# Performance work log

Hardware: AMD Instinct MI355X
Metric: run time of the kernel (lower is better)

Reference implementation:

```python
import jax, jax.numpy as jnp
import numpy as np

B, D, rL, rD, d = 512, 960, 16, 32, 512
LP, LH = 16, 384
R_PH = 0.7
dP = int(round(R_PH * d))  # 358
dH = d - dP                # 154
BN_EPS = 1e-5


def _xavier(key, shape):
    limit = float(np.sqrt(6.0 / (shape[0] + shape[1])))
    return jax.random.uniform(key, shape, jnp.float32, -limit, limit)


def _prefix_mask(key, batch, L_pad):
    # contiguous prefix masks: Lb uniform in [1, L_pad]
    lens = jax.random.randint(key, (batch,), 1, L_pad + 1)
    return (jnp.arange(L_pad)[None, :] < lens[:, None]).astype(jnp.int32)


def setup_inputs() -> dict:
    key = jax.random.key(0)
    ks = jax.random.split(key, 24)
    inp = {
        "emb_P": jax.random.normal(ks[0], (B, LP, D), jnp.float32),
        "emb_H": jax.random.normal(ks[1], (B, LH, D), jnp.float32),
        "mask_P": _prefix_mask(ks[2], B, LP),
        "mask_H": _prefix_mask(ks[3], B, LH),
        # peptide encoder params
        "B_cP": _xavier(ks[4], (D, rD)),
        "A_cP": _xavier(ks[5], (LP, rL)),
        "H_cP": _xavier(ks[6], (rL * rD, dP)),
        "W1P": _xavier(ks[7], (dP, dP)), "b1P": jnp.zeros((dP,), jnp.float32),
        "gP": jnp.ones((dP,), jnp.float32), "betaP": jnp.zeros((dP,), jnp.float32),
        "W2P": _xavier(ks[8], (dP, dP)), "b2P": jnp.zeros((dP,), jnp.float32),
        # HLA encoder params
        "B_cH": _xavier(ks[9], (D, rD)),
        "A_cH": _xavier(ks[10], (LH, rL)),
        "H_cH": _xavier(ks[11], (rL * rD, dH)),
        "W1H": _xavier(ks[12], (dH, dH)), "b1H": jnp.zeros((dH,), jnp.float32),
        "gH": jnp.ones((dH,), jnp.float32), "betaH": jnp.zeros((dH,), jnp.float32),
        "W2H": _xavier(ks[13], (dH, dH)), "b2H": jnp.zeros((dH,), jnp.float32),
    }
    return inp


def _encode(emb, mask, B_c, A_c, H_c, W1, b1, g, beta, W2, b2):
    # masked low-rank projection; equivalent to the per-sample ragged loop
    # for contiguous prefix masks (A_c rows align with padded positions).
    Xm = emb * mask[..., None].astype(emb.dtype)            # (B, L, D)
    Y = jnp.einsum("bld,dr->blr", Xm, B_c)                  # (B, L, rD)
    U = jnp.einsum("lp,blr->bpr", A_c, Y)                   # (B, rL, rD)
    z = U.reshape(U.shape[0], -1) @ H_c                     # (B, d_mod)
    # expander (eval mode: BN uses running stats mean=0/var=1; dropout off)
    h = z @ W1 + b1
    h = h * (g / jnp.sqrt(1.0 + BN_EPS)) + beta
    h = jax.nn.relu(h)
    return h @ W2 + b2


def reference(emb_P, emb_H, B_cP, A_cP, H_cP, W1P, b1P, gP, betaP, W2P, b2P,
              B_cH, A_cH, H_cH, W1H, b1H, gH, betaH, W2H, b2H,
              mask_P, mask_H):
    zP = _encode(emb_P, mask_P, B_cP, A_cP, H_cP, W1P, b1P, gP, betaP, W2P, b2P)
    zH = _encode(emb_H, mask_H, B_cH, A_cH, H_cH, W1H, b1H, gH, betaH, W2H, b2H)
    return jnp.concatenate([zP, zH], axis=-1)  # (B, d)
```

## Files before the change

kernel.cpp:

```cpp
#include <hip/hip_runtime.h>
#include <cstddef>

constexpr int Bn  = 512;
constexpr int Dd  = 960;
constexpr int RL  = 16;
constexpr int RD  = 32;
constexpr int LPp = 16;
constexpr int LHh = 384;
constexpr int DP  = 358;
constexpr int DH  = 154;

typedef float f32x4 __attribute__((ext_vector_type(4)));

struct EncParams {
    const float* X;
    const int*   mask;
    const float* A;
    const float* Bc;
    const float* Hc;
    const float* W1;
    const float* b1;
    const float* g;
    const float* beta;
    const float* W2;
    const float* b2;
    int L;
    int dmod;
    int ooff;
};

__global__ __launch_bounds__(256)
void fused_kernel(EncParams H, EncParams P, float* __restrict__ out)
{
    const bool isH = ((int)blockIdx.x < Bn);
    const EncParams E = isH ? H : P;
    const int b = isH ? blockIdx.x : blockIdx.x - Bn;
    const int t = threadIdx.x;

    __shared__ float Vs[RL][Dd];
    __shared__ float Ush[RL * RD];
    __shared__ int   s_len;

    if (t == 0) s_len = 0;
    __syncthreads();
    int loc = 0;
    for (int i = t; i < E.L; i += 256) loc += E.mask[(size_t)b * E.L + i];
    if (loc) atomicAdd(&s_len, loc);
    __syncthreads();
    const int len = s_len;

    if (t < 240) {
        float v[RL][4];
        #pragma unroll
        for (int p = 0; p < RL; ++p)
            #pragma unroll
            for (int q = 0; q < 4; ++q) v[p][q] = 0.f;

        const float* xrow = E.X + (size_t)b * E.L * Dd + 4 * t;
        #pragma unroll 2
        for (int l = 0; l < len; ++l) {
            f32x4 xv = __builtin_nontemporal_load((const f32x4*)xrow);
            xrow += Dd;
            float a[RL];
            *(f32x4*)&a[0]  = *(const f32x4*)(E.A + (size_t)l * RL + 0);
            *(f32x4*)&a[4]  = *(const f32x4*)(E.A + (size_t)l * RL + 4);
            *(f32x4*)&a[8]  = *(const f32x4*)(E.A + (size_t)l * RL + 8);
            *(f32x4*)&a[12] = *(const f32x4*)(E.A + (size_t)l * RL + 12);
            #pragma unroll
            for (int p = 0; p < RL; ++p) {
                v[p][0] = fmaf(a[p], xv[0], v[p][0]);
                v[p][1] = fmaf(a[p], xv[1], v[p][1]);
                v[p][2] = fmaf(a[p], xv[2], v[p][2]);
                v[p][3] = fmaf(a[p], xv[3], v[p][3]);
            }
        }
        #pragma unroll
        for (int p = 0; p < RL; ++p)
            *(f32x4*)&Vs[p][4 * t] = *(f32x4*)&v[p][0];
    }
    __syncthreads();

    {
        const int p = t >> 5, r = t & 31;
        float u0 = 0.f, u1 = 0.f;
        for (int dd = 0; dd < Dd; dd += 4) {
            f32x4 v0 = *(const f32x4*)&Vs[p][dd];
            f32x4 v1 = *(const f32x4*)&Vs[p + 8][dd];
            #pragma unroll
            for (int q = 0; q < 4; ++q) {
                float bc = E.Bc[(size_t)(dd + q) * RD + r];
                u0 = fmaf(v0[q], bc, u0);
                u1 = fmaf(v1[q], bc, u1);
            }
        }
        Ush[p * RD + r]       = u0;
        Ush[(p + 8) * RD + r] = u1;
    }
    __syncthreads();

    float* zs = &Vs[0][0];
    float* hs = &Vs[0][0] + 512;
    for (int j = t; j < E.dmod; j += 256) {
        float acc = 0.f;
        #pragma unroll 8
        for (int i = 0; i < RL * RD; ++i)
            acc = fmaf(Ush[i], E.Hc[(size_t)i * E.dmod + j], acc);
        zs[j] = acc;
    }
    __syncthreads();

    const float bscale = rsqrtf(1.f + 1e-5f);
    for (int c = t; c < E.dmod; c += 256) {
        float acc = E.b1[c];
        #pragma unroll 4
        for (int k = 0; k < E.dmod; ++k)
            acc = fmaf(zs[k], E.W1[(size_t)k * E.dmod + c], acc);
        acc = fmaf(acc, E.g[c] * bscale, E.beta[c]);
        hs[c] = fmaxf(acc, 0.f);
    }
    __syncthreads();

    for (int c = t; c < E.dmod; c += 256) {
        float acc = E.b2[c];
        #pragma unroll 4
        for (int k = 0; k < E.dmod; ++k)
            acc = fmaf(hs[k], E.W2[(size_t)k * E.dmod + c], acc);
        out[(size_t)b * (DP + DH) + E.ooff + c] = acc;
    }
}

extern "C" void kernel_launch(void* const* d_in, const int* in_sizes, int n_in,
                              void* d_out, int out_size, void* d_ws, size_t ws_size,
                              hipStream_t stream)
{
    EncParams P, H;
    P.X    = (const float*)d_in[0];
    H.X    = (const float*)d_in[1];
    P.mask = (const int*)  d_in[2];
    H.mask = (const int*)  d_in[3];
    P.Bc   = (const float*)d_in[4];
    P.A    = (const float*)d_in[5];
    P.Hc   = (const float*)d_in[6];
    P.W1   = (const float*)d_in[7];
    P.b1   = (const float*)d_in[8];
    P.g    = (const float*)d_in[9];
    P.beta = (const float*)d_in[10];
    P.W2   = (const float*)d_in[11];
    P.b2   = (const float*)d_in[12];
    H.Bc   = (const float*)d_in[13];
    H.A    = (const float*)d_in[14];
    H.Hc   = (const float*)d_in[15];
    H.W1   = (const float*)d_in[16];
    H.b1   = (const float*)d_in[17];
    H.g    = (const float*)d_in[18];
    H.beta = (const float*)d_in[19];
    H.W2   = (const float*)d_in[20];
    H.b2   = (const float*)d_in[21];
    P.L = LPp;  P.dmod = DP;  P.ooff = 0;
    H.L = LHh;  H.dmod = DH;  H.ooff = DP;

    float* outp = (float*)d_out;

    fused_kernel<<<dim3(2 * Bn), dim3(256), 0, stream>>>(H, P, outp);
}
```

Measured before the change: 249.2 us.

## Split sequence reduction into segmented kernel with workspace partials and tail kernel

```diff
diff --git a/kernel.cpp b/kernel.cpp
--- a/kernel.cpp
+++ b/kernel.cpp
@@ -9,36 +9,95 @@
 constexpr int LHh = 384;
 constexpr int DP  = 358;
 constexpr int DH  = 154;
+constexpr int SEGH  = 96;
+constexpr int NSEGH = 4;
 
 typedef float f32x4 __attribute__((ext_vector_type(4)));
 
-struct EncParams {
-    const float* X;
+__global__ __launch_bounds__(256)
+void vseg_kernel(const float* __restrict__ XH, const int* __restrict__ mH,
+                 const float* __restrict__ AH, float* __restrict__ VH,
+                 const float* __restrict__ XP, const int* __restrict__ mP,
+                 const float* __restrict__ AP, float* __restrict__ VP)
+{
+    const int id = blockIdx.x;
+    const float* X; const int* mask; const float* A; float* V;
+    int L, l0, seglen, b;
+    if (id < Bn * NSEGH) {
+        b = id >> 2; const int seg = id & 3;
+        X = XH; mask = mH; A = AH;
+        V = VH + (size_t)(b * NSEGH + seg) * RL * Dd;
+        L = LHh; l0 = seg * SEGH; seglen = SEGH;
+    } else {
+        b = id - Bn * NSEGH;
+        X = XP; mask = mP; A = AP;
+        V = VP + (size_t)b * RL * Dd;
+        L = LPp; l0 = 0; seglen = LPp;
+    }
+    const int t = threadIdx.x;
+
+    __shared__ int s_len;
+    if (t == 0) s_len = 0;
+    __syncthreads();
+    int loc = 0;
+    for (int i = t; i < L; i += 256) loc += mask[(size_t)b * L + i];
+    if (loc) atomicAdd(&s_len, loc);
+    __syncthreads();
+    const int len = __builtin_amdgcn_readfirstlane(s_len);
+
+    if (l0 >= len) return;
+    if (t >= 240) return;
+    const int l1 = min(len, l0 + seglen);
+
+    float v[RL][4];
+    #pragma unroll
+    for (int p = 0; p < RL; ++p)
+        #pragma unroll
+        for (int q = 0; q < 4; ++q) v[p][q] = 0.f;
+
+    const float* xrow = X + ((size_t)b * L + l0) * Dd + 4 * t;
+    for (int l = l0; l < l1; ++l) {
+        f32x4 xv = __builtin_nontemporal_load((const f32x4*)xrow);
+        xrow += Dd;
+        float a[RL];
+        *(f32x4*)&a[0]  = *(const f32x4*)(A + (size_t)l * RL + 0);
+        *(f32x4*)&a[4]  = *(const f32x4*)(A + (size_t)l * RL + 4);
+        *(f32x4*)&a[8]  = *(const f32x4*)(A + (size_t)l * RL + 8);
+        *(f32x4*)&a[12] = *(const f32x4*)(A + (size_t)l * RL + 12);
+        #pragma unroll
+        for (int p = 0; p < RL; ++p) {
+            v[p][0] = fmaf(a[p], xv[0], v[p][0]);
+            v[p][1] = fmaf(a[p], xv[1], v[p][1]);
+            v[p][2] = fmaf(a[p], xv[2], v[p][2]);
+            v[p][3] = fmaf(a[p], xv[3], v[p][3]);
+        }
+    }
+    #pragma unroll
+    for (int p = 0; p < RL; ++p)
+        *(f32x4*)(V + (size_t)p * Dd + 4 * t) = *(f32x4*)&v[p][0];
+}
+
+struct TailP {
     const int*   mask;
-    const float* A;
+    const float* V;
     const float* Bc;
     const float* Hc;
-    const float* W1;
-    const float* b1;
-    const float* g;
-    const float* beta;
-    const float* W2;
-    const float* b2;
-    int L;
-    int dmod;
-    int ooff;
+    const float* W1; const float* b1; const float* g; const float* beta;
+    const float* W2; const float* b2;
+    int L, dmod, ooff, max_segs, seglen;
 };
 
 __global__ __launch_bounds__(256)
-void fused_kernel(EncParams H, EncParams P, float* __restrict__ out)
+void tail_kernel(TailP H, TailP P, float* __restrict__ out)
 {
-    const bool isH = ((int)blockIdx.x < Bn);
-    const EncParams E = isH ? H : P;
-    const int b = isH ? blockIdx.x : blockIdx.x - Bn;
+    const bool isH = (blockIdx.x & 1);
+    const TailP E = isH ? H : P;
+    const int b = blockIdx.x >> 1;
     const int t = threadIdx.x;
 
-    __shared__ float Vs[RL][Dd];
     __shared__ float Ush[RL * RD];
+    __shared__ float zs[DP];
+    __shared__ float hs[DP];
     __shared__ int   s_len;
 
     if (t == 0) s_len = 0;
@@ -47,59 +106,29 @@
     for (int i = t; i < E.L; i += 256) loc += E.mask[(size_t)b * E.L + i];
     if (loc) atomicAdd(&s_len, loc);
     __syncthreads();
-    const int len = s_len;
-
-    if (t < 240) {
-        float v[RL][4];
-        #pragma unroll
-        for (int p = 0; p < RL; ++p)
-            #pragma unroll
-            for (int q = 0; q < 4; ++q) v[p][q] = 0.f;
-
-        const float* xrow = E.X + (size_t)b * E.L * Dd + 4 * t;
-        #pragma unroll 2
-        for (int l = 0; l < len; ++l) {
-            f32x4 xv = __builtin_nontemporal_load((const f32x4*)xrow);
-            xrow += Dd;
-            float a[RL];
-            *(f32x4*)&a[0]  = *(const f32x4*)(E.A + (size_t)l * RL + 0);
-            *(f32x4*)&a[4]  = *(const f32x4*)(E.A + (size_t)l * RL + 4);
-            *(f32x4*)&a[8]  = *(const f32x4*)(E.A + (size_t)l * RL + 8);
-            *(f32x4*)&a[12] = *(const f32x4*)(E.A + (size_t)l * RL + 12);
-            #pragma unroll
-            for (int p = 0; p < RL; ++p) {
-                v[p][0] = fmaf(a[p], xv[0], v[p][0]);
-                v[p][1] = fmaf(a[p], xv[1], v[p][1]);
-                v[p][2] = fmaf(a[p], xv[2], v[p][2]);
-                v[p][3] = fmaf(a[p], xv[3], v[p][3]);
-            }
+    const int len  = __builtin_amdgcn_readfirstlane(s_len);
+    const int nseg = min(E.max_segs, (len + E.seglen - 1) / E.seglen);
+
+    const float* Vb = E.V + (size_t)b * E.max_segs * RL * Dd;
+    const int p = t >> 5, r = t & 31;
+    float u0 = 0.f, u1 = 0.f;
+    for (int d = 0; d < Dd; d += 4) {
+        f32x4 a0 = {0.f, 0.f, 0.f, 0.f}, a1 = {0.f, 0.f, 0.f, 0.f};
+        for (int s = 0; s < nseg; ++s) {
+            a0 += *(const f32x4*)(Vb + ((size_t)s * RL + p) * Dd + d);
+            a1 += *(const f32x4*)(Vb + ((size_t)s * RL + p + 8) * Dd + d);
         }
         #pragma unroll
-        for (int p = 0; p < RL; ++p)
-            *(f32x4*)&Vs[p][4 * t] = *(f32x4*)&v[p][0];
-    }
-    __syncthreads();
-
-    {
-        const int p = t >> 5, r = t & 31;
-        float u0 = 0.f, u1 = 0.f;
-        for (int dd = 0; dd < Dd; dd += 4) {
-            f32x4 v0 = *(const f32x4*)&Vs[p][dd];
-            f32x4 v1 = *(const f32x4*)&Vs[p + 8][dd];
-            #pragma unroll
-            for (int q = 0; q < 4; ++q) {
-                float bc = E.Bc[(size_t)(dd + q) * RD + r];
-                u0 = fmaf(v0[q], bc, u0);
-                u1 = fmaf(v1[q], bc, u1);
-            }
+        for (int q = 0; q < 4; ++q) {
+            float bc = E.Bc[(size_t)(d + q) * RD + r];
+            u0 = fmaf(a0[q], bc, u0);
+            u1 = fmaf(a1[q], bc, u1);
         }
-        Ush[p * RD + r]       = u0;
-        Ush[(p + 8) * RD + r] = u1;
-    }
-    __syncthreads();
-
-    float* zs = &Vs[0][0];
-    float* hs = &Vs[0][0] + 512;
+    }
+    Ush[p * RD + r]       = u0;
+    Ush[(p + 8) * RD + r] = u1;
+    __syncthreads();
+
     for (int j = t; j < E.dmod; j += 256) {
         float acc = 0.f;
         #pragma unroll 8
@@ -133,33 +162,48 @@
                               void* d_out, int out_size, void* d_ws, size_t ws_size,
                               hipStream_t stream)
 {
-    EncParams P, H;
-    P.X    = (const float*)d_in[0];
-    H.X    = (const float*)d_in[1];
-    P.mask = (const int*)  d_in[2];
-    H.mask = (const int*)  d_in[3];
-    P.Bc   = (const float*)d_in[4];
-    P.A    = (const float*)d_in[5];
-    P.Hc   = (const float*)d_in[6];
-    P.W1   = (const float*)d_in[7];
-    P.b1   = (const float*)d_in[8];
-    P.g    = (const float*)d_in[9];
-    P.beta = (const float*)d_in[10];
-    P.W2   = (const float*)d_in[11];
-    P.b2   = (const float*)d_in[12];
-    H.Bc   = (const float*)d_in[13];
-    H.A    = (const float*)d_in[14];
-    H.Hc   = (const float*)d_in[15];
-    H.W1   = (const float*)d_in[16];
-    H.b1   = (const float*)d_in[17];
-    H.g    = (const float*)d_in[18];
-    H.beta = (const float*)d_in[19];
-    H.W2   = (const float*)d_in[20];
-    H.b2   = (const float*)d_in[21];
-    P.L = LPp;  P.dmod = DP;  P.ooff = 0;
-    H.L = LHh;  H.dmod = DH;  H.ooff = DP;
-
+    const float* emb_P  = (const float*)d_in[0];
+    const float* emb_H  = (const float*)d_in[1];
+    const int*   mask_P = (const int*)  d_in[2];
+    const int*   mask_H = (const int*)  d_in[3];
+    const float* B_cP   = (const float*)d_in[4];
+    const float* A_cP   = (const float*)d_in[5];
+    const float* H_cP   = (const float*)d_in[6];
+    const float* W1P    = (const float*)d_in[7];
+    const float* b1P    = (const float*)d_in[8];
+    const float* gP     = (const float*)d_in[9];
+    const float* betaP  = (const float*)d_in[10];
+    const float* W2P    = (const float*)d_in[11];
+    const float* b2P    = (const float*)d_in[12];
+    const float* B_cH   = (const float*)d_in[13];
+    const float* A_cH   = (const float*)d_in[14];
+    const float* H_cH   = (const float*)d_in[15];
+    const float* W1H    = (const float*)d_in[16];
+    const float* b1H    = (const float*)d_in[17];
+    const float* gH     = (const float*)d_in[18];
+    const float* betaH  = (const float*)d_in[19];
+    const float* W2H    = (const float*)d_in[20];
+    const float* b2H    = (const float*)d_in[21];
     float* outp = (float*)d_out;
 
-    fused_kernel<<<dim3(2 * Bn), dim3(256), 0, stream>>>(H, P, outp);
+    float* ws  = (float*)d_ws;
+    float* V_H = ws;
+    float* V_P = V_H + (size_t)Bn * NSEGH * RL * Dd;
+
+    dim3 blk(256);
+
+    vseg_kernel<<<dim3(Bn * NSEGH + Bn), blk, 0, stream>>>(
+        emb_H, mask_H, A_cH, V_H,
+        emb_P, mask_P, A_cP, V_P);
+
+    TailP H, P;
+    H.mask = mask_H; H.V = V_H; H.Bc = B_cH; H.Hc = H_cH;
+    H.W1 = W1H; H.b1 = b1H; H.g = gH; H.beta = betaH; H.W2 = W2H; H.b2 = b2H;
+    H.L = LHh; H.dmod = DH; H.ooff = DP; H.max_segs = NSEGH; H.seglen = SEGH;
+
+    P.mask = mask_P; P.V = V_P; P.Bc = B_cP; P.Hc = H_cP;
+    P.W1 = W1P; P.b1 = b1P; P.g = gP; P.beta = betaP; P.W2 = W2P; P.b2 = b2P;
+    P.L = LPp; P.dmod = DP; P.ooff = 0; P.max_segs = 1; P.seglen = LPp;
+
+    tail_kernel<<<dim3(2 * Bn), blk, 0, stream>>>(H, P, outp);
 }
```

Result: slower. 457.9 us (+83.8%).

## Convert to persistent kernel with atomic work queue over samples

Applied to the files above, without the earlier changes.

```diff
diff --git a/kernel.cpp b/kernel.cpp
--- a/kernel.cpp
+++ b/kernel.cpp
@@ -18,114 +18,144 @@
     const float* A;
     const float* Bc;
     const float* Hc;
-    const float* W1;
-    const float* b1;
-    const float* g;
-    const float* beta;
-    const float* W2;
-    const float* b2;
-    int L;
-    int dmod;
-    int ooff;
+    const float* W1; const float* b1; const float* g; const float* beta;
+    const float* W2; const float* b2;
+    int L, dmod, ooff;
 };
 
+__global__ void zero_kernel(int* __restrict__ q)
+{
+    if (threadIdx.x == 0) *q = 0;
+}
+
 __global__ __launch_bounds__(256)
-void fused_kernel(EncParams H, EncParams P, float* __restrict__ out)
+void persist_kernel(EncParams H, EncParams P, int* __restrict__ qcnt,
+                    float* __restrict__ out)
 {
-    const bool isH = ((int)blockIdx.x < Bn);
-    const EncParams E = isH ? H : P;
-    const int b = isH ? blockIdx.x : blockIdx.x - Bn;
     const int t = threadIdx.x;
-
     __shared__ float Vs[RL][Dd];
     __shared__ float Ush[RL * RD];
-    __shared__ int   s_len;
+    __shared__ int   s_item, s_len;
 
-    if (t == 0) s_len = 0;
-    __syncthreads();
-    int loc = 0;
-    for (int i = t; i < E.L; i += 256) loc += E.mask[(size_t)b * E.L + i];
-    if (loc) atomicAdd(&s_len, loc);
-    __syncthreads();
-    const int len = s_len;
+    for (;;) {
+        __syncthreads();
+        if (t == 0) { s_item = atomicAdd(qcnt, 1); s_len = 0; }
+        __syncthreads();
+        const int item = s_item;
+        if (item >= 2 * Bn) return;
+        const bool isH = (item < Bn);
+        const EncParams E = isH ? H : P;
+        const int b = isH ? item : item - Bn;
 
-    if (t < 240) {
-        float v[RL][4];
-        #pragma unroll
-        for (int p = 0; p < RL; ++p)
+        int loc = 0;
+        for (int i = t; i < E.L; i += 256) loc += E.mask[(size_t)b * E.L + i];
+        if (loc) atomicAdd(&s_len, loc);
+        __syncthreads();
+        const int len = s_len;
+
+        if (t < 240) {
+            float v[RL][4];
             #pragma unroll
-            for (int q = 0; q < 4; ++q) v[p][q] = 0.f;
+            for (int p = 0; p < RL; ++p)
+                #pragma unroll
+                for (int q = 0; q < 4; ++q) v[p][q] = 0.f;
 
-        const float* xrow = E.X + (size_t)b * E.L * Dd + 4 * t;
-        #pragma unroll 2
-        for (int l = 0; l < len; ++l) {
-            f32x4 xv = __builtin_nontemporal_load((const f32x4*)xrow);
-            xrow += Dd;
-            float a[RL];
-            *(f32x4*)&a[0]  = *(const f32x4*)(E.A + (size_t)l * RL + 0);
-            *(f32x4*)&a[4]  = *(const f32x4*)(E.A + (size_t)l * RL + 4);
-            *(f32x4*)&a[8]  = *(const f32x4*)(E.A + (size_t)l * RL + 8);
-            *(f32x4*)&a[12] = *(const f32x4*)(E.A + (size_t)l * RL + 12);
+            const float* xrow = E.X + (size_t)b * E.L * Dd + 4 * t;
+            int l = 0;
+            for (; l + 1 < len; l += 2) {
+                f32x4 xv0 = __builtin_nontemporal_load((const f32x4*)xrow);
+                f32x4 xv1 = __builtin_nontemporal_load((const f32x4*)(xrow + Dd));
+                xrow += 2 * Dd;
+                float a0[RL], a1[RL];
+                *(f32x4*)&a0[0]  = *(const f32x4*)(E.A + (size_t)l * RL + 0);
+                *(f32x4*)&a0[4]  = *(const f32x4*)(E.A + (size_t)l * RL + 4);
+                *(f32x4*)&a0[8]  = *(const f32x4*)(E.A + (size_t)l * RL + 8);
+                *(f32x4*)&a0[12] = *(const f32x4*)(E.A + (size_t)l * RL + 12);
+                *(f32x4*)&a1[0]  = *(const f32x4*)(E.A + (size_t)(l + 1) * RL + 0);
+                *(f32x4*)&a1[4]  = *(const f32x4*)(E.A + (size_t)(l + 1) * RL + 4);
+                *(f32x4*)&a1[8]  = *(const f32x4*)(E.A + (size_t)(l + 1) * RL + 8);
+                *(f32x4*)&a1[12] = *(const f32x4*)(E.A + (size_t)(l + 1) * RL + 12);
+                #pragma unroll
+                for (int p = 0; p < RL; ++p) {
+                    #pragma unroll
+                    for (int q = 0; q < 4; ++q)
+                        v[p][q] = fmaf(a0[p], xv0[q], v[p][q]);
+                }
+                #pragma unroll
+                for (int p = 0; p < RL; ++p) {
+                    #pragma unroll
+                    for (int q = 0; q < 4; ++q)
+                        v[p][q] = fmaf(a1[p], xv1[q], v[p][q]);
+                }
+            }
+            if (l < len) {
+                f32x4 xv = __builtin_nontemporal_load((const f32x4*)xrow);
+                float a[RL];
+                *(f32x4*)&a[0]  = *(const f32x4*)(E.A + (size_t)l * RL + 0);
+                *(f32x4*)&a[4]  = *(const f32x4*)(E.A + (size_t)l * RL + 4);
+                *(f32x4*)&a[8]  = *(const f32x4*)(E.A + (size_t)l * RL + 8);
+                *(f32x4*)&a[12] = *(const f32x4*)(E.A + (size_t)l * RL + 12);
+                #pragma unroll
+                for (int p = 0; p < RL; ++p)
+                    #pragma unroll
+                    for (int q = 0; q < 4; ++q)
+                        v[p][q] = fmaf(a[p], xv[q], v[p][q]);
+            }
             #pragma unroll
-            for (int p = 0; p < RL; ++p) {
-                v[p][0] = fmaf(a[p], xv[0], v[p][0]);
-                v[p][1] = fmaf(a[p], xv[1], v[p][1]);
-                v[p][2] = fmaf(a[p], xv[2], v[p][2]);
-                v[p][3] = fmaf(a[p], xv[3], v[p][3]);
+            for (int p = 0; p < RL; ++p)
+                *(f32x4*)&Vs[p][4 * t] = *(f32x4*)&v[p][0];
+        }
+        __syncthreads();
+
+        {
+            const int p = t >> 5, r = t & 31;
+            float u0 = 0.f, u1 = 0.f;
+            for (int dd = 0; dd < Dd; dd += 4) {
+                f32x4 v0 = *(const f32x4*)&Vs[p][dd];
+                f32x4 v1 = *(const f32x4*)&Vs[p + 8][dd];
+                #pragma unroll
+                for (int q = 0; q < 4; ++q) {
+                    float bc = E.Bc[(size_t)(dd + q) * RD + r];
+                    u0 = fmaf(v0[q], bc, u0);
+                    u1 = fmaf(v1[q], bc, u1);
+                }
             }
+            Ush[p * RD + r]       = u0;
+            Ush[(p + 8) * RD + r] = u1;
         }
-        #pragma unroll
-        for (int p = 0; p < RL; ++p)
-            *(f32x4*)&Vs[p][4 * t] = *(f32x4*)&v[p][0];
-    }
-    __syncthreads();
+        __syncthreads();
 
-    {
-        const int p = t >> 5, r = t & 31;
-        float u0 = 0.f, u1 = 0.f;
-        for (int dd = 0; dd < Dd; dd += 4) {
-            f32x4 v0 = *(const f32x4*)&Vs[p][dd];
-            f32x4 v1 = *(const f32x4*)&Vs[p + 8][dd];
-            #pragma unroll
-            for (int q = 0; q < 4; ++q) {
-                float bc = E.Bc[(size_t)(dd + q) * RD + r];
-                u0 = fmaf(v0[q], bc, u0);
-                u1 = fmaf(v1[q], bc, u1);
+        float* zs = &Vs[0][0];
+        float* hs = &Vs[0][0] + 512;
+        for (int j = t; j < E.dmod; j += 256) {
+            float acc0 = 0.f, acc1 = 0.f;
+            #pragma unroll 8
+            for (int i = 0; i < RL * RD; i += 2) {
+                acc0 = fmaf(Ush[i],     E.Hc[(size_t)i * E.dmod + j],       acc0);
+                acc1 = fmaf(Ush[i + 1], E.Hc[(size_t)(i + 1) * E.dmod + j], acc1);
             }
+            zs[j] = acc0 + acc1;
         }
-        Ush[p * RD + r]       = u0;
-        Ush[(p + 8) * RD + r] = u1;
-    }
-    __syncthreads();
+        __syncthreads();
 
-    float* zs = &Vs[0][0];
-    float* hs = &Vs[0][0] + 512;
-    for (int j = t; j < E.dmod; j += 256) {
-        float acc = 0.f;
-        #pragma unroll 8
-        for (int i = 0; i < RL * RD; ++i)
-            acc = fmaf(Ush[i], E.Hc[(size_t)i * E.dmod + j], acc);
-        zs[j] = acc;
-    }
-    __syncthreads();
+        const float bscale = rsqrtf(1.f + 1e-5f);
+        for (int c = t; c < E.dmod; c += 256) {
+            float acc = E.b1[c];
+            #pragma unroll 4
+            for (int k = 0; k < E.dmod; ++k)
+                acc = fmaf(zs[k], E.W1[(size_t)k * E.dmod + c], acc);
+            acc = fmaf(acc, E.g[c] * bscale, E.beta[c]);
+            hs[c] = fmaxf(acc, 0.f);
+        }
+        __syncthreads();
 
-    const float bscale = rsqrtf(1.f + 1e-5f);
-    for (int c = t; c < E.dmod; c += 256) {
-        float acc = E.b1[c];
-        #pragma unroll 4
-        for (int k = 0; k < E.dmod; ++k)
-            acc = fmaf(zs[k], E.W1[(size_t)k * E.dmod + c], acc);
-        acc = fmaf(acc, E.g[c] * bscale, E.beta[c]);
-        hs[c] = fmaxf(acc, 0.f);
-    }
-    __syncthreads();
-
-    for (int c = t; c < E.dmod; c += 256) {
-        float acc = E.b2[c];
-        #pragma unroll 4
-        for (int k = 0; k < E.dmod; ++k)
-            acc = fmaf(hs[k], E.W2[(size_t)k * E.dmod + c], acc);
-        out[(size_t)b * (DP + DH) + E.ooff + c] = acc;
+        for (int c = t; c < E.dmod; c += 256) {
+            float acc = E.b2[c];
+            #pragma unroll 4
+            for (int k = 0; k < E.dmod; ++k)
+                acc = fmaf(hs[k], E.W2[(size_t)k * E.dmod + c], acc);
+            out[(size_t)b * (DP + DH) + E.ooff + c] = acc;
+        }
     }
 }
 
@@ -160,6 +190,8 @@
     H.L = LHh;  H.dmod = DH;  H.ooff = DP;
 
     float* outp = (float*)d_out;
+    int*   qcnt = (int*)d_ws;
 
-    fused_kernel<<<dim3(2 * Bn), dim3(256), 0, stream>>>(H, P, outp);
+    zero_kernel<<<dim3(1), dim3(64), 0, stream>>>(qcnt);
+    persist_kernel<<<dim3(512), dim3(256), 0, stream>>>(H, P, qcnt, outp);
 }
```

New measurement: 256.2 us. 1.03x slower.
